# Kernel tuning notes

Measured on AMD Instinct MI355X. Metric: run time of the kernel, lower is better.

## Reference

```python
import jax, jax.numpy as jnp
import numpy as np

# ---- static config (seq_lens / is_prefill are Python lists in the original) ----
HIDDEN, H, D = 4096, 32, 128
SEQ = 1024            # prefill length / decode history length
N_PRE, N_DEC = 4, 4
T = N_PRE * SEQ + N_DEC            # 4100 total tokens
SEQ_LENS = [SEQ] * N_PRE + [SEQ] * N_DEC
IS_PREFILL = [True] * N_PRE + [False] * N_DEC
NUM_SLOTS = 8192
MAX_LEN, ROPE_BASE = 8192, 10000.0
SCALE = D ** -0.5


def _rope_tables():
    inv_freq = 1.0 / (ROPE_BASE ** (np.arange(0, D, 2, dtype=np.float32) / D))
    t = np.arange(MAX_LEN, dtype=np.float32)
    freqs = np.outer(t, inv_freq)
    emb = np.concatenate([freqs, freqs], axis=-1)  # [MAX_LEN, D]
    return jnp.asarray(np.cos(emb), jnp.float32), jnp.asarray(np.sin(emb), jnp.float32)

COS_T, SIN_T = _rope_tables()


def rotate_half(x):
    x1, x2 = jnp.split(x, 2, axis=-1)
    return jnp.concatenate([-x2, x1], axis=-1)


def setup_inputs() -> dict:
    key = jax.random.key(0)
    k1, k2, k3 = jax.random.split(key, 3)
    x = jax.random.normal(k1, (T, HIDDEN), jnp.float32)
    # positions: prefill seqs get 0..SEQ-1, decode seqs are at position SEQ
    pos = np.concatenate([np.tile(np.arange(SEQ), N_PRE), np.full(N_DEC, SEQ)]).astype(np.int64)
    positions = jnp.asarray(pos)
    slot_mapping = jnp.arange(T, dtype=jnp.int64)
    k_cache = jnp.zeros((NUM_SLOTS, H, D), jnp.float32)
    v_cache = jnp.zeros((NUM_SLOTS, H, D), jnp.float32)
    w_qkv = jax.random.normal(k2, (HIDDEN, 3 * H * D), jnp.float32) * 0.02
    w_out = jax.random.normal(k3, (H * D, HIDDEN), jnp.float32) * 0.02
    return {"x": x, "k_cache": k_cache, "v_cache": v_cache, "w_qkv": w_qkv,
            "w_out": w_out, "positions": positions, "slot_mapping": slot_mapping}


def reference(x, k_cache, v_cache, w_qkv, w_out, positions, slot_mapping):
    qkv = x @ w_qkv                                   # [T, 3*H*D]
    q, k, v = jnp.split(qkv, 3, axis=-1)
    q = q.reshape(T, H, D)
    k = k.reshape(T, H, D)
    v = v.reshape(T, H, D)
    cos = COS_T[positions][:, None, :]                # [T, 1, D]
    sin = SIN_T[positions][:, None, :]
    q = q * cos + rotate_half(q) * sin
    k = k * cos + rotate_half(k) * sin
    # scatter new k/v into flat paged cache
    kc = k_cache.at[slot_mapping].set(k)
    vc = v_cache.at[slot_mapping].set(v)

    outs = []
    off = 0
    for seq_len, prefill in zip(SEQ_LENS, IS_PREFILL):
        nq = seq_len if prefill else 1
        q_i = q[off:off + nq]                         # [nq, H, D]
        if prefill:
            k_i, v_i = k[off:off + nq], v[off:off + nq]
            attn = jnp.einsum('qhd,khd->hqk', q_i, k_i) * SCALE
            mask = jnp.triu(jnp.full((nq, nq), -jnp.inf, jnp.float32), 1)
            attn = jax.nn.softmax(attn + mask, axis=-1)
            out = jnp.einsum('hqk,khd->qhd', attn, v_i).reshape(nq, H * D)
        else:
            k_h, v_h = kc[:seq_len], vc[:seq_len]     # history from cache
            attn = jnp.einsum('qhd,khd->hqk', q_i, k_h) * SCALE
            attn = jax.nn.softmax(attn, axis=-1)
            out = jnp.einsum('hqk,khd->qhd', attn, v_h).reshape(1, H * D)
        outs.append(out)
        off += nq
    return jnp.concatenate(outs, axis=0) @ w_out      # [T, HIDDEN]
```

## Files before the change

### kernel.cpp

```cpp
#include <hip/hip_runtime.h>

#define T_TOK 4100
#define MMAIN 4096
#define HID   4096
#define NH    32
#define DH    128
#define NQKV  12288
#define ATT_SCALE 0.08838834764831845f
#define NEG_BIG  (-3.0e38f)

typedef unsigned short ushort_t;
typedef __attribute__((ext_vector_type(8))) short bf16x8;
typedef __attribute__((ext_vector_type(4))) float f32x4;

typedef const void __attribute__((address_space(1)))* gas_ptr;
typedef void __attribute__((address_space(3)))* las_ptr;

__device__ __forceinline__ ushort_t f2bf(float f){
  unsigned int u = __builtin_bit_cast(unsigned int, f);
  u = u + 0x7FFFu + ((u >> 16) & 1u);
  return (ushort_t)(u >> 16);
}
__device__ __forceinline__ float bf2f(ushort_t h){
  unsigned int u = ((unsigned int)h) << 16;
  return __builtin_bit_cast(float, u);
}
__device__ __forceinline__ f32x4 mfma16(bf16x8 a, bf16x8 b, f32x4 c){
  return __builtin_amdgcn_mfma_f32_16x16x32_bf16(a, b, c, 0, 0, 0);
}
__device__ __forceinline__ void gload_lds16(const void* g, void* l){
  __builtin_amdgcn_global_load_lds((gas_ptr)g, (las_ptr)l, 16, 0, 0);
}


__global__ void convert_x(const float* __restrict__ x, ushort_t* __restrict__ xb){
  const long i4 = (long)blockIdx.x * 256 + threadIdx.x;
  if (i4 >= (long)T_TOK * HID / 4) return;
  const long i = i4 * 4;
  const float4 v = *(const float4*)(x + i);
  union { ushort_t u[4]; uint2 w; } o;
  o.u[0] = f2bf(v.x); o.u[1] = f2bf(v.y); o.u[2] = f2bf(v.z); o.u[3] = f2bf(v.w);
  *(uint2*)(xb + i) = o.w;
}

__global__ void tconv(const float* __restrict__ W, ushort_t* __restrict__ WT, int R, int C){
  __shared__ float tile[32][33];
  const int bc = blockIdx.x, br = blockIdx.y;
  const int tid = threadIdx.x;
  const int cl = tid & 31, rl = tid >> 5;
  const long c = (long)bc * 32 + cl;
#pragma unroll
  for (int j = 0; j < 32; j += 8)
    tile[rl + j][cl] = W[((long)br * 32 + rl + j) * C + c];
  __syncthreads();
#pragma unroll
  for (int j = 0; j < 32; j += 8)
    WT[((long)bc * 32 + rl + j) * R + (long)br * 32 + cl] = f2bf(tile[cl][rl + j]);
}


#define MFMAQ(QM,QN,BARR)                                                         \
  _Pragma("unroll")                                                               \
  for (int mi = 0; mi < 4; ++mi) {                                                \
    _Pragma("unroll")                                                             \
    for (int ni = 0; ni < 2; ++ni) {                                              \
      acc[QM][QN][mi][ni] = mfma16(af[mi][0], BARR[ni][0], acc[QM][QN][mi][ni]);  \
      acc[QM][QN][mi][ni] = mfma16(af[mi][1], BARR[ni][1], acc[QM][QN][mi][ni]);  \
    } }

template<bool OUT_BF16>
__global__ void __launch_bounds__(512, 2)
gemm256(const ushort_t* __restrict__ A, const ushort_t* __restrict__ B,
        ushort_t* __restrict__ Cb, float* __restrict__ Cf,
        int N, int K, int GM, int Mvalid)
{
  extern __shared__ char smem[];
  char* smA = smem;
  char* smB = smem + 65536;

  const int nwg = gridDim.x;
  int bid = blockIdx.x;
  bid = (bid & 7) * (nwg >> 3) + (bid >> 3);
  const int bm = bid % GM, bn = bid / GM;

  const int tid = threadIdx.x;
  const int wid = tid >> 6, lane = tid & 63;
  const int wm = wid >> 2, wn = wid & 3;
  const int l16 = lane & 15, g = lane >> 4;
  const int lr = lane >> 3, lu = lane & 7;

  const long arow0 = (long)bm * 256;
  const long brow0 = (long)bn * 256;

  const ushort_t* aS[4]; const ushort_t* bS[4];
#pragma unroll
  for (int cc = 0; cc < 4; ++cc){
    aS[cc] = A + (arow0 + cc*64 + wid*8 + lr) * (long)K + (lu ^ lr) * 8;
    bS[cc] = B + (brow0 + cc*64 + wid*8 + lr) * (long)K + (lu ^ lr) * 8;
  }

  auto stageA = [&](int buf, int cc, long kt){
    gload_lds16(aS[cc] + kt, smA + buf*32768 + (cc*64 + wid*8)*128);
  };
  auto stageB = [&](int buf, int cc, long kt){
    gload_lds16(bS[cc] + kt, smB + buf*32768 + (cc*64 + wid*8)*128);
  };
  auto ldA = [&](int buf, int qm, int mi, int ks) -> bf16x8 {
    const int row = qm*128 + wm*64 + mi*16 + l16;
    return *(const bf16x8*)(smA + buf*32768 + row*128 + (((ks*4+g) ^ (l16&7))*16));
  };
  auto ldB = [&](int buf, int qn, int ni, int ks) -> bf16x8 {
    const int row = qn*128 + wn*32 + ni*16 + l16;
    return *(const bf16x8*)(smB + buf*32768 + row*128 + (((ks*4+g) ^ (l16&7))*16));
  };

  f32x4 acc[2][2][4][2];
#pragma unroll
  for (int a_ = 0; a_ < 2; ++a_)
#pragma unroll
  for (int b_ = 0; b_ < 2; ++b_)
#pragma unroll
  for (int c_ = 0; c_ < 4; ++c_)
#pragma unroll
  for (int d_ = 0; d_ < 2; ++d_) acc[a_][b_][c_][d_] = (f32x4){0.f,0.f,0.f,0.f};

  bf16x8 af[4][2], bf0[2][2], bf1[2][2];
  const int NT = K >> 6;

  stageA(0,0,0); stageA(0,1,0);
  stageB(0,0,0); stageB(0,1,0);
  stageB(0,2,0); stageB(0,3,0);
  stageA(0,2,0); stageA(0,3,0);
  asm volatile("s_waitcnt vmcnt(4)" ::: "memory");
  __builtin_amdgcn_s_barrier();

  auto tile = [&](int buf, long ktn){
    asm volatile("s_waitcnt vmcnt(2)" ::: "memory");
#pragma unroll
    for (int mi = 0; mi < 4; ++mi){ af[mi][0] = ldA(buf,0,mi,0); af[mi][1] = ldA(buf,0,mi,1); }
#pragma unroll
    for (int ni = 0; ni < 2; ++ni){ bf0[ni][0] = ldB(buf,0,ni,0); bf0[ni][1] = ldB(buf,0,ni,1); }
    stageA(buf^1, 0, ktn); stageA(buf^1, 1, ktn);
    __builtin_amdgcn_s_barrier();
    asm volatile("s_waitcnt lgkmcnt(0)" ::: "memory");
    __builtin_amdgcn_sched_barrier(0);
    __builtin_amdgcn_s_setprio(1);
    MFMAQ(0,0,bf0);
    __builtin_amdgcn_s_setprio(0);
    asm volatile("s_waitcnt vmcnt(2)" ::: "memory");
#pragma unroll
    for (int ni = 0; ni < 2; ++ni){ bf1[ni][0] = ldB(buf,1,ni,0); bf1[ni][1] = ldB(buf,1,ni,1); }
    stageB(buf^1, 0, ktn); stageB(buf^1, 1, ktn);
    __builtin_amdgcn_s_barrier();
    asm volatile("s_waitcnt lgkmcnt(0)" ::: "memory");
    __builtin_amdgcn_sched_barrier(0);
    __builtin_amdgcn_s_setprio(1);
    MFMAQ(0,1,bf1);
    __builtin_amdgcn_s_setprio(0);
#pragma unroll
    for (int mi = 0; mi < 4; ++mi){ af[mi][0] = ldA(buf,1,mi,0); af[mi][1] = ldA(buf,1,mi,1); }
    stageB(buf^1, 2, ktn); stageB(buf^1, 3, ktn);
    __builtin_amdgcn_s_barrier();
    asm volatile("s_waitcnt lgkmcnt(0)" ::: "memory");
    __builtin_amdgcn_sched_barrier(0);
    __builtin_amdgcn_s_setprio(1);
    MFMAQ(1,1,bf1);
    __builtin_amdgcn_s_setprio(0);
    asm volatile("s_waitcnt vmcnt(2)" ::: "memory");
    stageA(buf^1, 2, ktn); stageA(buf^1, 3, ktn);
    __builtin_amdgcn_s_barrier();
    __builtin_amdgcn_sched_barrier(0);
    __builtin_amdgcn_s_setprio(1);
    MFMAQ(1,0,bf0);
    __builtin_amdgcn_s_setprio(0);
  };

  for (int t = 0; t < NT; t += 2){
    const long k1 = (long)(t+1) * 64;
    const long k2 = (long)((t+2 < NT) ? (t+2) : (NT-1)) * 64;
    tile(0, k1);
    tile(1, k2);
  }
  asm volatile("s_waitcnt vmcnt(0)" ::: "memory");

#pragma unroll
  for (int qm = 0; qm < 2; ++qm)
#pragma unroll
  for (int qn = 0; qn < 2; ++qn)
#pragma unroll
  for (int mi = 0; mi < 4; ++mi)
#pragma unroll
  for (int ni = 0; ni < 2; ++ni)
#pragma unroll
  for (int r = 0; r < 4; ++r){
    const long row = arow0 + qm*128 + wm*64 + mi*16 + g*4 + r;
    const long col = brow0 + qn*128 + wn*32 + ni*16 + l16;
    if (OUT_BF16){
      Cb[row * N + col] = f2bf(acc[qm][qn][mi][ni][r]);
    } else {
      if (row < Mvalid) Cf[row * N + col] = acc[qm][qn][mi][ni][r];
    }
  }
}


__global__ void __launch_bounds__(256, 8)
gemv_tail(const ushort_t* __restrict__ A, const ushort_t* __restrict__ B,
          ushort_t* __restrict__ Cb, float* __restrict__ Cf, int ldc)
{
  const int col  = blockIdx.x * 4 + (threadIdx.x >> 6);
  const int lane = threadIdx.x & 63;
  const ushort_t* brow  = B + (long)col * HID + lane * 64;
  const ushort_t* abase = A + 4096L * HID + lane * 64;
  float acc0 = 0.f, acc1 = 0.f, acc2 = 0.f, acc3 = 0.f;
#pragma unroll
  for (int i = 0; i < 8; ++i){
    union { bf16x8 v; short s[8]; } bv, a0, a1, a2, a3;
    bv.v = *(const bf16x8*)(brow + i*8);
    a0.v = *(const bf16x8*)(abase + 0L*HID + i*8);
    a1.v = *(const bf16x8*)(abase + 1L*HID + i*8);
    a2.v = *(const bf16x8*)(abase + 2L*HID + i*8);
    a3.v = *(const bf16x8*)(abase + 3L*HID + i*8);
#pragma unroll
    for (int e = 0; e < 8; ++e){
      const float bf_ = bf2f((ushort_t)bv.s[e]);
      acc0 += bf2f((ushort_t)a0.s[e]) * bf_;
      acc1 += bf2f((ushort_t)a1.s[e]) * bf_;
      acc2 += bf2f((ushort_t)a2.s[e]) * bf_;
      acc3 += bf2f((ushort_t)a3.s[e]) * bf_;
    }
  }
#pragma unroll
  for (int off = 32; off; off >>= 1){
    acc0 += __shfl_xor(acc0, off);
    acc1 += __shfl_xor(acc1, off);
    acc2 += __shfl_xor(acc2, off);
    acc3 += __shfl_xor(acc3, off);
  }
  if (lane == 0){
    if (Cb){
      Cb[4096L*ldc + col] = f2bf(acc0);
      Cb[4097L*ldc + col] = f2bf(acc1);
      Cb[4098L*ldc + col] = f2bf(acc2);
      Cb[4099L*ldc + col] = f2bf(acc3);
    } else {
      Cf[4096L*ldc + col] = acc0;
      Cf[4097L*ldc + col] = acc1;
      Cf[4098L*ldc + col] = acc2;
      Cf[4099L*ldc + col] = acc3;
    }
  }
}


__global__ void rope_scatter(ushort_t* __restrict__ qkv,
                             const int* __restrict__ pos32,
                             const int* __restrict__ slot32,
                             ushort_t* __restrict__ kcw, ushort_t* __restrict__ vcw)
{
  const long gi = (long)blockIdx.x * 256 + threadIdx.x;
  if (gi >= (long)T_TOK * NH * 64) return;
  const int  i = gi & 63;
  const int  h = (gi >> 6) & 31;
  const long t = gi >> 11;

  const bool p64 = (pos32[1] == 0);
  const bool s64 = (slot32[1] == 0);
  const long pv   = p64 ? ((const long long*)pos32)[t]  : (long)pos32[t];
  const long slot = s64 ? ((const long long*)slot32)[t] : (long)slot32[t];

  const float inv = exp2f(-(float)i * 0.2076187116f);
  const float ang = (float)pv * inv;
  float sn, cs;
  __sincosf(ang, &sn, &cs);

  ushort_t* base = qkv + t * (long)NQKV + h * DH + i;
  const float q1 = bf2f(base[0]), q2 = bf2f(base[64]);
  base[0]  = f2bf(q1 * cs - q2 * sn);
  base[64] = f2bf(q2 * cs + q1 * sn);

  if (t < 4096){
    ushort_t* kb = base + HID;
    const float k1 = bf2f(kb[0]), k2 = bf2f(kb[64]);
    const float k1n = k1 * cs - k2 * sn, k2n = k2 * cs + k1 * sn;
    kb[0]  = f2bf(k1n);
    kb[64] = f2bf(k2n);

    if (slot >= 0 && slot < 1024){
      ushort_t* kd = kcw + (slot * NH + h) * DH + i;
      kd[0] = f2bf(k1n); kd[64] = f2bf(k2n);
      const ushort_t* vsrc = base + 2 * HID;
      ushort_t* vd = vcw + (slot * NH + h) * DH + i;
      vd[0] = vsrc[0]; vd[64] = vsrc[64];
    }
  }
}


__global__ void __launch_bounds__(256, 3)
attn_fused(const ushort_t* __restrict__ qkv, const ushort_t* __restrict__ kcw,
           const ushort_t* __restrict__ vcw, ushort_t* __restrict__ attn)
{
  __shared__ char sm[44032];
  const int qb = blockIdx.x, h = blockIdx.y, sq = blockIdx.z;
  const int tid = threadIdx.x, wid = tid >> 6, lane = tid & 63;

  if (qb == 16){
    float* qs  = (float*)sm;
    float* ps  = qs + 128;
    float* red = ps + 1024;
    float* oh  = red + 8;
    const long t = 4096 + sq;
    if (tid < 128) qs[tid] = bf2f(qkv[t * (long)NQKV + h*DH + tid]);
    __syncthreads();
    float sv[4];
#pragma unroll
    for (int j = 0; j < 4; j++){
      const int key = tid + j*256;
      const ushort_t* kr = kcw + ((long)key * NH + h) * DH;
      float acc = 0.f;
      for (int d = 0; d < 128; d += 8){
        union { bf16x8 v; short s[8]; } uu;
        uu.v = *(const bf16x8*)(kr + d);
#pragma unroll
        for (int e = 0; e < 8; e++) acc += qs[d+e] * bf2f((ushort_t)uu.s[e]);
      }
      sv[j] = acc * ATT_SCALE;
    }
    float mx = fmaxf(fmaxf(sv[0], sv[1]), fmaxf(sv[2], sv[3]));
#pragma unroll
    for (int off = 1; off < 64; off <<= 1) mx = fmaxf(mx, __shfl_xor(mx, off));
    if (lane == 0) red[wid] = mx;
    __syncthreads();
    const float gmax = fmaxf(fmaxf(red[0], red[1]), fmaxf(red[2], red[3]));
    float psum = 0.f;
#pragma unroll
    for (int j = 0; j < 4; j++){
      const float p = __expf(sv[j] - gmax);
      ps[tid + j*256] = p;
      psum += p;
    }
#pragma unroll
    for (int off = 1; off < 64; off <<= 1) psum += __shfl_xor(psum, off);
    if (lane == 0) red[4 + wid] = psum;
    __syncthreads();
    const float gsum = red[4] + red[5] + red[6] + red[7];
    const int d = tid & 127, half = tid >> 7;
    float acc = 0.f;
    for (int key = half*512; key < half*512 + 512; ++key)
      acc += ps[key] * bf2f(vcw[((long)key * NH + h) * DH + d]);
    if (half) oh[d] = acc;
    __syncthreads();
    if (!half) attn[t * HID + h*DH + d] = f2bf((acc + oh[d]) / gsum);
    return;
  }

  ushort_t (*Ks)[128]    = (ushort_t(*)[128])sm;
  ushort_t (*Vt)[72]     = (ushort_t(*)[72])(sm + 16384);
  ushort_t (*Ps)[16][72] = (ushort_t(*)[16][72])(sm + 34816);
  const long tok0 = (long)sq * 1024;
  const int l16 = lane & 15, g = lane >> 4;
  const int q0 = qb * 64;

  bf16x8 qf[4];
  {
    const ushort_t* qrow = qkv + (tok0 + q0 + wid*16 + l16) * (long)NQKV + h * DH;
#pragma unroll
    for (int dc = 0; dc < 4; ++dc) qf[dc] = *(const bf16x8*)(qrow + dc*32 + g*8);
  }

  f32x4 oacc[8];
#pragma unroll
  for (int i = 0; i < 8; i++) oacc[i] = (f32x4){0.f, 0.f, 0.f, 0.f};
  float mrow[4] = {NEG_BIG, NEG_BIG, NEG_BIG, NEG_BIG};
  float lrow[4] = {0.f, 0.f, 0.f, 0.f};

  const int nkb = qb + 1;
  for (int kb = 0; kb < nkb; ++kb){
    __syncthreads();
    {
      const ushort_t* kbase = qkv + (tok0 + kb*64) * (long)NQKV + HID + h * DH;
#pragma unroll
      for (int c = 0; c < 4; ++c){
        const int row = c*16 + wid*4 + g;
        const int pu = (l16 & 8) | ((l16 ^ (row & 7)) & 7);
        gload_lds16(kbase + (long)row * NQKV + pu*8, &Ks[c*16 + wid*4][0]);
      }
    }
    {
      const int key4 = (tid & 15) * 4;
      const int dg8  = tid >> 4;
      const ushort_t* vbase = qkv + (tok0 + kb*64) * (long)NQKV + 2*HID + h*DH + dg8*8;
      union { bf16x8 v; short s[8]; } vr[4];
#pragma unroll
      for (int j = 0; j < 4; ++j)
        vr[j].v = *(const bf16x8*)(vbase + (long)(key4 + j) * NQKV);
#pragma unroll
      for (int e = 0; e < 8; ++e){
        union { ushort_t u[4]; uint2 w; } o;
        o.u[0] = (ushort_t)vr[0].s[e]; o.u[1] = (ushort_t)vr[1].s[e];
        o.u[2] = (ushort_t)vr[2].s[e]; o.u[3] = (ushort_t)vr[3].s[e];
        *(uint2*)&Vt[dg8*8 + e][key4] = o.w;
      }
    }
    __syncthreads();

    {
      f32x4 sfr[4];
#pragma unroll
      for (int nf = 0; nf < 4; ++nf) sfr[nf] = (f32x4){0.f,0.f,0.f,0.f};
#pragma unroll
      for (int nf = 0; nf < 4; ++nf){
#pragma unroll
        for (int dc = 0; dc < 4; ++dc){
          const int uu = dc*4 + g;
          const int pu = (uu & 8) | ((uu ^ (l16 & 7)) & 7);
          bf16x8 kf = *(const bf16x8*)&Ks[nf*16 + l16][pu * 8];
          sfr[nf] = mfma16(qf[dc], kf, sfr[nf]);
        }
      }
      const bool diag = (kb == qb);
      float alpha[4];
#pragma unroll
      for (int r = 0; r < 4; r++){
        float s[4];
#pragma unroll
        for (int nf = 0; nf < 4; ++nf) s[nf] = sfr[nf][r] * ATT_SCALE;
        if (diag){
          const int qg = q0 + wid*16 + g*4 + r;
#pragma unroll
          for (int nf = 0; nf < 4; ++nf)
            if (kb*64 + nf*16 + l16 > qg) s[nf] = NEG_BIG;
        }
        float mx = fmaxf(fmaxf(s[0], s[1]), fmaxf(s[2], s[3]));
        mx = fmaxf(mx, __shfl_xor(mx, 1));
        mx = fmaxf(mx, __shfl_xor(mx, 2));
        mx = fmaxf(mx, __shfl_xor(mx, 4));
        mx = fmaxf(mx, __shfl_xor(mx, 8));
        const float mn = fmaxf(mrow[r], mx);
        const float al = __expf(mrow[r] - mn);
        float p[4], rs = 0.f;
#pragma unroll
        for (int nf = 0; nf < 4; ++nf){ p[nf] = __expf(s[nf] - mn); rs += p[nf]; }
        rs += __shfl_xor(rs, 1);
        rs += __shfl_xor(rs, 2);
        rs += __shfl_xor(rs, 4);
        rs += __shfl_xor(rs, 8);
        lrow[r] = lrow[r] * al + rs;
        mrow[r] = mn;
        alpha[r] = al;
#pragma unroll
        for (int nf = 0; nf < 4; ++nf)
          Ps[wid][g*4 + r][nf*16 + l16] = f2bf(p[nf]);
      }
#pragma unroll
      for (int df = 0; df < 8; ++df){
        f32x4 o = oacc[df];
        o[0] *= alpha[0]; o[1] *= alpha[1]; o[2] *= alpha[2]; o[3] *= alpha[3];
        oacc[df] = o;
      }
#pragma unroll
      for (int ks = 0; ks < 2; ++ks){
        bf16x8 pa = *(const bf16x8*)&Ps[wid][l16][ks*32 + g*8];
#pragma unroll
        for (int df = 0; df < 8; ++df){
          bf16x8 vf = *(const bf16x8*)&Vt[df*16 + l16][ks*32 + g*8];
          oacc[df] = mfma16(pa, vf, oacc[df]);
        }
      }
    }
  }

#pragma unroll
  for (int df = 0; df < 8; ++df){
#pragma unroll
    for (int r = 0; r < 4; ++r){
      const long row = tok0 + q0 + wid*16 + g*4 + r;
      attn[row * HID + h*DH + df*16 + l16] = f2bf(oacc[df][r] / lrow[r]);
    }
  }
}


extern "C" void kernel_launch(void* const* d_in, const int* in_sizes, int n_in,
                              void* d_out, int out_size, void* d_ws, size_t ws_size,
                              hipStream_t stream) {
  const float* x      = (const float*)d_in[0];
  const float* wqkv   = (const float*)d_in[3];
  const float* wout   = (const float*)d_in[4];
  const int*   pos    = (const int*)d_in[5];
  const int*   slots  = (const int*)d_in[6];

  char* ws = (char*)d_ws;
  ushort_t* xb    = (ushort_t*)(ws);
  ushort_t* qkvb  = (ushort_t*)(ws + 35651584L);
  ushort_t* wqkvT = (ushort_t*)(ws + 142606336L);
  ushort_t* attnb = (ushort_t*)(ws + 142606336L);
  ushort_t* woutT = (ushort_t*)(ws + 243269632L);
  ushort_t* kcw   = (ushort_t*)(ws + 276824064L);
  ushort_t* vcw   = (ushort_t*)(ws + 285212672L);

  hipFuncSetAttribute((const void*)gemm256<true>,
                      hipFuncAttributeMaxDynamicSharedMemorySize, 131072);
  hipFuncSetAttribute((const void*)gemm256<false>,
                      hipFuncAttributeMaxDynamicSharedMemorySize, 131072);

  convert_x<<<16400, 256, 0, stream>>>(x, xb);
  tconv<<<dim3(NQKV/32, HID/32), 256, 0, stream>>>(wqkv, wqkvT, HID, NQKV);
  tconv<<<dim3(HID/32, HID/32), 256, 0, stream>>>(wout, woutT, HID, HID);

  gemm256<true><<<(MMAIN/256)*(NQKV/256), 512, 131072, stream>>>(
      xb, wqkvT, qkvb, nullptr, NQKV, HID, MMAIN/256, MMAIN);
  gemv_tail<<<HID/4, 256, 0, stream>>>(xb, wqkvT, qkvb, nullptr, NQKV);

  rope_scatter<<<32800, 256, 0, stream>>>(qkvb, pos, slots, kcw, vcw);

  attn_fused<<<dim3(17, NH, 4), 256, 0, stream>>>(qkvb, kcw, vcw, attnb);

  gemm256<false><<<(MMAIN/256)*(HID/256), 512, 131072, stream>>>(
      attnb, woutT, nullptr, (float*)d_out, HID, HID, MMAIN/256, MMAIN);
  gemv_tail<<<HID/4, 256, 0, stream>>>(attnb, woutT, nullptr, (float*)d_out, HID);

  (void)in_sizes; (void)n_in; (void)out_size; (void)ws_size;
}
```

Baseline: 837.3 us.

## Double-buffer K/V tiles in attention and schedule longest query blocks first

The prefill attention loop now double-buffers K and V tiles in shared memory. The next tile's K is loaded asynchronously into LDS and its V is held in registers while the current tile's MFMAs run, which cuts the loop to one barrier per iteration. Query blocks are reversed (qb = 15 - bx) so the blocks with the most causal work are dispatched first, to reduce tail imbalance. The kernel moves to dynamic shared memory of about 77 KB and launch bounds drop from 3 to 2 blocks per CU, trading occupancy for overlap.

Result: no change. 847.9 us (+1.3%).

```diff
diff --git a/kernel.cpp b/kernel.cpp
--- a/kernel.cpp
+++ b/kernel.cpp
@@ -297,15 +297,15 @@
 }
 
 
-__global__ void __launch_bounds__(256, 3)
+__global__ void __launch_bounds__(256, 2)
 attn_fused(const ushort_t* __restrict__ qkv, const ushort_t* __restrict__ kcw,
            const ushort_t* __restrict__ vcw, ushort_t* __restrict__ attn)
 {
-  __shared__ char sm[44032];
-  const int qb = blockIdx.x, h = blockIdx.y, sq = blockIdx.z;
+  extern __shared__ char sm[];
+  const int bx = blockIdx.x, h = blockIdx.y, sq = blockIdx.z;
   const int tid = threadIdx.x, wid = tid >> 6, lane = tid & 63;
 
-  if (qb == 16){
+  if (bx == 16){
     float* qs  = (float*)sm;
     float* ps  = qs + 128;
     float* red = ps + 1024;
@@ -355,12 +355,14 @@
     return;
   }
 
-  ushort_t (*Ks)[128]    = (ushort_t(*)[128])sm;
-  ushort_t (*Vt)[72]     = (ushort_t(*)[72])(sm + 16384);
-  ushort_t (*Ps)[16][72] = (ushort_t(*)[16][72])(sm + 34816);
+  char* smKs = sm;
+  char* smVt = sm + 32768;
+  char* smPs = sm + 69632;
+  const int qb = 15 - bx;
   const long tok0 = (long)sq * 1024;
   const int l16 = lane & 15, g = lane >> 4;
   const int q0 = qb * 64;
+  const int key4 = (tid & 15) * 4, dg8 = tid >> 4;
 
   bf16x8 qf[4];
   {
@@ -369,106 +371,115 @@
     for (int dc = 0; dc < 4; ++dc) qf[dc] = *(const bf16x8*)(qrow + dc*32 + g*8);
   }
 
+  auto Kstage = [&](int kb, int buf){
+    const ushort_t* kbase = qkv + (tok0 + kb*64) * (long)NQKV + HID + h * DH;
+#pragma unroll
+    for (int c = 0; c < 4; ++c){
+      const int row = c*16 + wid*4 + g;
+      const int pu = (l16 & 8) | ((l16 ^ (row & 7)) & 7);
+      gload_lds16(kbase + (long)row * NQKV + pu*8, smKs + buf*16384 + (c*16 + wid*4)*256);
+    }
+  };
+  bf16x8 vreg[4];
+  auto Vload = [&](int kb){
+    const ushort_t* vbase = qkv + (tok0 + kb*64) * (long)NQKV + 2*HID + h*DH + dg8*8;
+#pragma unroll
+    for (int j = 0; j < 4; ++j)
+      vreg[j] = *(const bf16x8*)(vbase + (long)(key4 + j) * NQKV);
+  };
+  auto Vwrite = [&](int buf){
+    union { bf16x8 v; short s[8]; } vr[4];
+#pragma unroll
+    for (int j = 0; j < 4; ++j) vr[j].v = vreg[j];
+#pragma unroll
+    for (int e = 0; e < 8; ++e){
+      union { ushort_t u[4]; uint2 w; } o;
+      o.u[0] = (ushort_t)vr[0].s[e]; o.u[1] = (ushort_t)vr[1].s[e];
+      o.u[2] = (ushort_t)vr[2].s[e]; o.u[3] = (ushort_t)vr[3].s[e];
+      *(uint2*)(smVt + buf*18432 + ((dg8*8 + e)*72 + key4)*2) = o.w;
+    }
+  };
+
   f32x4 oacc[8];
 #pragma unroll
   for (int i = 0; i < 8; i++) oacc[i] = (f32x4){0.f, 0.f, 0.f, 0.f};
   float mrow[4] = {NEG_BIG, NEG_BIG, NEG_BIG, NEG_BIG};
   float lrow[4] = {0.f, 0.f, 0.f, 0.f};
 
-  const int nkb = qb + 1;
-  for (int kb = 0; kb < nkb; ++kb){
+  Kstage(0, 0);
+  Vload(0);
+  Vwrite(0);
+  __syncthreads();
+
+  for (int kb = 0; kb <= qb; ++kb){
+    const int buf = kb & 1;
+    if (kb < qb){ Kstage(kb + 1, buf ^ 1); Vload(kb + 1); }
+
+    f32x4 sfr[4];
+#pragma unroll
+    for (int nf = 0; nf < 4; ++nf) sfr[nf] = (f32x4){0.f,0.f,0.f,0.f};
+#pragma unroll
+    for (int nf = 0; nf < 4; ++nf){
+#pragma unroll
+      for (int dc = 0; dc < 4; ++dc){
+        const int uu = dc*4 + g;
+        const int pu = (uu & 8) | ((uu ^ (l16 & 7)) & 7);
+        bf16x8 kf = *(const bf16x8*)(smKs + buf*16384 + (nf*16 + l16)*256 + pu*16);
+        sfr[nf] = mfma16(qf[dc], kf, sfr[nf]);
+      }
+    }
+    const bool diag = (kb == qb);
+    float alpha[4];
+#pragma unroll
+    for (int r = 0; r < 4; r++){
+      float s[4];
+#pragma unroll
+      for (int nf = 0; nf < 4; ++nf) s[nf] = sfr[nf][r] * ATT_SCALE;
+      if (diag){
+        const int qg = q0 + wid*16 + g*4 + r;
+#pragma unroll
+        for (int nf = 0; nf < 4; ++nf)
+          if (kb*64 + nf*16 + l16 > qg) s[nf] = NEG_BIG;
+      }
+      float mx = fmaxf(fmaxf(s[0], s[1]), fmaxf(s[2], s[3]));
+      mx = fmaxf(mx, __shfl_xor(mx, 1));
+      mx = fmaxf(mx, __shfl_xor(mx, 2));
+      mx = fmaxf(mx, __shfl_xor(mx, 4));
+      mx = fmaxf(mx, __shfl_xor(mx, 8));
+      const float mn = fmaxf(mrow[r], mx);
+      const float al = __expf(mrow[r] - mn);
+      float p[4], rs = 0.f;
+#pragma unroll
+      for (int nf = 0; nf < 4; ++nf){ p[nf] = __expf(s[nf] - mn); rs += p[nf]; }
+      rs += __shfl_xor(rs, 1);
+      rs += __shfl_xor(rs, 2);
+      rs += __shfl_xor(rs, 4);
+      rs += __shfl_xor(rs, 8);
+      lrow[r] = lrow[r] * al + rs;
+      mrow[r] = mn;
+      alpha[r] = al;
+#pragma unroll
+      for (int nf = 0; nf < 4; ++nf)
+        *(ushort_t*)(smPs + ((wid*16 + g*4 + r)*72 + nf*16 + l16)*2) = f2bf(p[nf]);
+    }
+#pragma unroll
+    for (int df = 0; df < 8; ++df){
+      f32x4 o = oacc[df];
+      o[0] *= alpha[0]; o[1] *= alpha[1]; o[2] *= alpha[2]; o[3] *= alpha[3];
+      oacc[df] = o;
+    }
+#pragma unroll
+    for (int ks = 0; ks < 2; ++ks){
+      bf16x8 pa = *(const bf16x8*)(smPs + ((wid*16 + l16)*72 + ks*32 + g*8)*2);
+#pragma unroll
+      for (int df = 0; df < 8; ++df){
+        bf16x8 vf = *(const bf16x8*)(smVt + buf*18432 + ((df*16 + l16)*72 + ks*32 + g*8)*2);
+        oacc[df] = mfma16(pa, vf, oacc[df]);
+      }
+    }
+
+    if (kb < qb) Vwrite(buf ^ 1);
     __syncthreads();
-    {
-      const ushort_t* kbase = qkv + (tok0 + kb*64) * (long)NQKV + HID + h * DH;
-#pragma unroll
-      for (int c = 0; c < 4; ++c){
-        const int row = c*16 + wid*4 + g;
-        const int pu = (l16 & 8) | ((l16 ^ (row & 7)) & 7);
-        gload_lds16(kbase + (long)row * NQKV + pu*8, &Ks[c*16 + wid*4][0]);
-      }
-    }
-    {
-      const int key4 = (tid & 15) * 4;
-      const int dg8  = tid >> 4;
-      const ushort_t* vbase = qkv + (tok0 + kb*64) * (long)NQKV + 2*HID + h*DH + dg8*8;
-      union { bf16x8 v; short s[8]; } vr[4];
-#pragma unroll
-      for (int j = 0; j < 4; ++j)
-        vr[j].v = *(const bf16x8*)(vbase + (long)(key4 + j) * NQKV);
-#pragma unroll
-      for (int e = 0; e < 8; ++e){
-        union { ushort_t u[4]; uint2 w; } o;
-        o.u[0] = (ushort_t)vr[0].s[e]; o.u[1] = (ushort_t)vr[1].s[e];
-        o.u[2] = (ushort_t)vr[2].s[e]; o.u[3] = (ushort_t)vr[3].s[e];
-        *(uint2*)&Vt[dg8*8 + e][key4] = o.w;
-      }
-    }
-    __syncthreads();
-
-    {
-      f32x4 sfr[4];
-#pragma unroll
-      for (int nf = 0; nf < 4; ++nf) sfr[nf] = (f32x4){0.f,0.f,0.f,0.f};
-#pragma unroll
-      for (int nf = 0; nf < 4; ++nf){
-#pragma unroll
-        for (int dc = 0; dc < 4; ++dc){
-          const int uu = dc*4 + g;
-          const int pu = (uu & 8) | ((uu ^ (l16 & 7)) & 7);
-          bf16x8 kf = *(const bf16x8*)&Ks[nf*16 + l16][pu * 8];
-          sfr[nf] = mfma16(qf[dc], kf, sfr[nf]);
-        }
-      }
-      const bool diag = (kb == qb);
-      float alpha[4];
-#pragma unroll
-      for (int r = 0; r < 4; r++){
-        float s[4];
-#pragma unroll
-        for (int nf = 0; nf < 4; ++nf) s[nf] = sfr[nf][r] * ATT_SCALE;
-        if (diag){
-          const int qg = q0 + wid*16 + g*4 + r;
-#pragma unroll
-          for (int nf = 0; nf < 4; ++nf)
-            if (kb*64 + nf*16 + l16 > qg) s[nf] = NEG_BIG;
-        }
-        float mx = fmaxf(fmaxf(s[0], s[1]), fmaxf(s[2], s[3]));
-        mx = fmaxf(mx, __shfl_xor(mx, 1));
-        mx = fmaxf(mx, __shfl_xor(mx, 2));
-        mx = fmaxf(mx, __shfl_xor(mx, 4));
-        mx = fmaxf(mx, __shfl_xor(mx, 8));
-        const float mn = fmaxf(mrow[r], mx);
-        const float al = __expf(mrow[r] - mn);
-        float p[4], rs = 0.f;
-#pragma unroll
-        for (int nf = 0; nf < 4; ++nf){ p[nf] = __expf(s[nf] - mn); rs += p[nf]; }
-        rs += __shfl_xor(rs, 1);
-        rs += __shfl_xor(rs, 2);
-        rs += __shfl_xor(rs, 4);
-        rs += __shfl_xor(rs, 8);
-        lrow[r] = lrow[r] * al + rs;
-        mrow[r] = mn;
-        alpha[r] = al;
-#pragma unroll
-        for (int nf = 0; nf < 4; ++nf)
-          Ps[wid][g*4 + r][nf*16 + l16] = f2bf(p[nf]);
-      }
-#pragma unroll
-      for (int df = 0; df < 8; ++df){
-        f32x4 o = oacc[df];
-        o[0] *= alpha[0]; o[1] *= alpha[1]; o[2] *= alpha[2]; o[3] *= alpha[3];
-        oacc[df] = o;
-      }
-#pragma unroll
-      for (int ks = 0; ks < 2; ++ks){
-        bf16x8 pa = *(const bf16x8*)&Ps[wid][l16][ks*32 + g*8];
-#pragma unroll
-        for (int df = 0; df < 8; ++df){
-          bf16x8 vf = *(const bf16x8*)&Vt[df*16 + l16][ks*32 + g*8];
-          oacc[df] = mfma16(pa, vf, oacc[df]);
-        }
-      }
-    }
   }
 
 #pragma unroll
@@ -504,6 +515,8 @@
                       hipFuncAttributeMaxDynamicSharedMemorySize, 131072);
   hipFuncSetAttribute((const void*)gemm256<false>,
                       hipFuncAttributeMaxDynamicSharedMemorySize, 131072);
+  hipFuncSetAttribute((const void*)attn_fused,
+                      hipFuncAttributeMaxDynamicSharedMemorySize, 78848);
 
   convert_x<<<16400, 256, 0, stream>>>(x, xb);
   tconv<<<dim3(NQKV/32, HID/32), 256, 0, stream>>>(wqkv, wqkvT, HID, NQKV);
@@ -515,7 +528,7 @@
 
   rope_scatter<<<32800, 256, 0, stream>>>(qkvb, pos, slots, kcw, vcw);
 
-  attn_fused<<<dim3(17, NH, 4), 256, 0, stream>>>(qkvb, kcw, vcw, attnb);
+  attn_fused<<<dim3(17, NH, 4), 256, 78848, stream>>>(qkvb, kcw, vcw, attnb);
 
   gemm256<false><<<(MMAIN/256)*(HID/256), 512, 131072, stream>>>(
       attnb, woutT, nullptr, (float*)d_out, HID, HID, MMAIN/256, MMAIN);
```

## Widen attention query tile to 128 rows with 512-thread blocks and K/V reuse

Applied to the files above, without the earlier changes.

The prefill attention kernel now processes 128 query rows per block with 8 waves, so each staged 64-key K/V tile is shared by twice as many queries, roughly halving global K/V loads. Blocks are launched in reverse (heaviest-first) order, waves skip key tiles entirely above their causal diagonal, and s_setprio is raised around the MFMA sections. Shared memory becomes dynamic and sized for the larger P buffer. The decode path is adapted to 512 threads. The trade-offs are lower occupancy, idle waves on diagonal tiles, and fewer blocks in the grid.

Result: slower. 870.7 us (+4.0%).

```diff
diff --git a/kernel.cpp b/kernel.cpp
--- a/kernel.cpp
+++ b/kernel.cpp
@@ -297,26 +297,26 @@
 }
 
 
-__global__ void __launch_bounds__(256, 3)
+__global__ void __launch_bounds__(512, 2)
 attn_fused(const ushort_t* __restrict__ qkv, const ushort_t* __restrict__ kcw,
            const ushort_t* __restrict__ vcw, ushort_t* __restrict__ attn)
 {
-  __shared__ char sm[44032];
-  const int qb = blockIdx.x, h = blockIdx.y, sq = blockIdx.z;
+  extern __shared__ char sm[];
+  const int bx = blockIdx.x, h = blockIdx.y, sq = blockIdx.z;
   const int tid = threadIdx.x, wid = tid >> 6, lane = tid & 63;
 
-  if (qb == 16){
+  if (bx == 8){
     float* qs  = (float*)sm;
     float* ps  = qs + 128;
     float* red = ps + 1024;
-    float* oh  = red + 8;
+    float* oh  = red + 16;
     const long t = 4096 + sq;
     if (tid < 128) qs[tid] = bf2f(qkv[t * (long)NQKV + h*DH + tid]);
     __syncthreads();
-    float sv[4];
-#pragma unroll
-    for (int j = 0; j < 4; j++){
-      const int key = tid + j*256;
+    float sv[2];
+#pragma unroll
+    for (int j = 0; j < 2; j++){
+      const int key = tid + j*512;
       const ushort_t* kr = kcw + ((long)key * NH + h) * DH;
       float acc = 0.f;
       for (int d = 0; d < 128; d += 8){
@@ -327,44 +327,51 @@
       }
       sv[j] = acc * ATT_SCALE;
     }
-    float mx = fmaxf(fmaxf(sv[0], sv[1]), fmaxf(sv[2], sv[3]));
+    float mx = fmaxf(sv[0], sv[1]);
 #pragma unroll
     for (int off = 1; off < 64; off <<= 1) mx = fmaxf(mx, __shfl_xor(mx, off));
     if (lane == 0) red[wid] = mx;
     __syncthreads();
-    const float gmax = fmaxf(fmaxf(red[0], red[1]), fmaxf(red[2], red[3]));
+    float gmax = red[0];
+#pragma unroll
+    for (int w = 1; w < 8; ++w) gmax = fmaxf(gmax, red[w]);
     float psum = 0.f;
 #pragma unroll
-    for (int j = 0; j < 4; j++){
+    for (int j = 0; j < 2; j++){
       const float p = __expf(sv[j] - gmax);
-      ps[tid + j*256] = p;
+      ps[tid + j*512] = p;
       psum += p;
     }
 #pragma unroll
     for (int off = 1; off < 64; off <<= 1) psum += __shfl_xor(psum, off);
-    if (lane == 0) red[4 + wid] = psum;
+    if (lane == 0) red[8 + wid] = psum;
     __syncthreads();
-    const float gsum = red[4] + red[5] + red[6] + red[7];
-    const int d = tid & 127, half = tid >> 7;
+    float gsum = red[8];
+#pragma unroll
+    for (int w = 1; w < 8; ++w) gsum += red[8 + w];
+    const int d = tid & 127, q4 = tid >> 7;
     float acc = 0.f;
-    for (int key = half*512; key < half*512 + 512; ++key)
+    for (int key = q4*256; key < q4*256 + 256; ++key)
       acc += ps[key] * bf2f(vcw[((long)key * NH + h) * DH + d]);
-    if (half) oh[d] = acc;
+    if (q4) oh[(q4-1)*128 + d] = acc;
     __syncthreads();
-    if (!half) attn[t * HID + h*DH + d] = f2bf((acc + oh[d]) / gsum);
+    if (!q4) attn[t * HID + h*DH + d] = f2bf((acc + oh[d] + oh[128+d] + oh[256+d]) / gsum);
     return;
   }
 
-  ushort_t (*Ks)[128]    = (ushort_t(*)[128])sm;
-  ushort_t (*Vt)[72]     = (ushort_t(*)[72])(sm + 16384);
-  ushort_t (*Ps)[16][72] = (ushort_t(*)[16][72])(sm + 34816);
+  char* smKs = sm;
+  char* smVt = sm + 16384;
+  char* smPs = sm + 34816;
+  const int qb = 7 - bx;
   const long tok0 = (long)sq * 1024;
   const int l16 = lane & 15, g = lane >> 4;
-  const int q0 = qb * 64;
+  const int q0 = qb * 128;
+  const int q0w = q0 + wid*16;
+  const int key2 = (tid & 31) * 2, dg8 = tid >> 5;
 
   bf16x8 qf[4];
   {
-    const ushort_t* qrow = qkv + (tok0 + q0 + wid*16 + l16) * (long)NQKV + h * DH;
+    const ushort_t* qrow = qkv + (tok0 + q0w + l16) * (long)NQKV + h * DH;
 #pragma unroll
     for (int dc = 0; dc < 4; ++dc) qf[dc] = *(const bf16x8*)(qrow + dc*32 + g*8);
   }
@@ -375,51 +382,50 @@
   float mrow[4] = {NEG_BIG, NEG_BIG, NEG_BIG, NEG_BIG};
   float lrow[4] = {0.f, 0.f, 0.f, 0.f};
 
-  const int nkb = qb + 1;
+  const int nkb = 2*qb + 2;
   for (int kb = 0; kb < nkb; ++kb){
     __syncthreads();
     {
       const ushort_t* kbase = qkv + (tok0 + kb*64) * (long)NQKV + HID + h * DH;
 #pragma unroll
-      for (int c = 0; c < 4; ++c){
-        const int row = c*16 + wid*4 + g;
+      for (int c = 0; c < 2; ++c){
+        const int row = c*32 + wid*4 + g;
         const int pu = (l16 & 8) | ((l16 ^ (row & 7)) & 7);
-        gload_lds16(kbase + (long)row * NQKV + pu*8, &Ks[c*16 + wid*4][0]);
+        gload_lds16(kbase + (long)row * NQKV + pu*8, smKs + (c*32 + wid*4)*256);
       }
     }
     {
-      const int key4 = (tid & 15) * 4;
-      const int dg8  = tid >> 4;
       const ushort_t* vbase = qkv + (tok0 + kb*64) * (long)NQKV + 2*HID + h*DH + dg8*8;
-      union { bf16x8 v; short s[8]; } vr[4];
-#pragma unroll
-      for (int j = 0; j < 4; ++j)
-        vr[j].v = *(const bf16x8*)(vbase + (long)(key4 + j) * NQKV);
+      union { bf16x8 v; short s[8]; } vr[2];
+#pragma unroll
+      for (int j = 0; j < 2; ++j)
+        vr[j].v = *(const bf16x8*)(vbase + (long)(key2 + j) * NQKV);
 #pragma unroll
       for (int e = 0; e < 8; ++e){
-        union { ushort_t u[4]; uint2 w; } o;
+        union { ushort_t u[2]; unsigned w; } o;
         o.u[0] = (ushort_t)vr[0].s[e]; o.u[1] = (ushort_t)vr[1].s[e];
-        o.u[2] = (ushort_t)vr[2].s[e]; o.u[3] = (ushort_t)vr[3].s[e];
-        *(uint2*)&Vt[dg8*8 + e][key4] = o.w;
+        *(unsigned*)(smVt + ((dg8*8 + e)*72 + key2)*2) = o.w;
       }
     }
     __syncthreads();
 
-    {
+    if (kb*64 <= q0w + 15){
       f32x4 sfr[4];
 #pragma unroll
       for (int nf = 0; nf < 4; ++nf) sfr[nf] = (f32x4){0.f,0.f,0.f,0.f};
+      __builtin_amdgcn_s_setprio(1);
 #pragma unroll
       for (int nf = 0; nf < 4; ++nf){
 #pragma unroll
         for (int dc = 0; dc < 4; ++dc){
           const int uu = dc*4 + g;
           const int pu = (uu & 8) | ((uu ^ (l16 & 7)) & 7);
-          bf16x8 kf = *(const bf16x8*)&Ks[nf*16 + l16][pu * 8];
+          bf16x8 kf = *(const bf16x8*)(smKs + (nf*16 + l16)*256 + pu*16);
           sfr[nf] = mfma16(qf[dc], kf, sfr[nf]);
         }
       }
-      const bool diag = (kb == qb);
+      __builtin_amdgcn_s_setprio(0);
+      const bool diag = (kb*64 + 63 > q0w);
       float alpha[4];
 #pragma unroll
       for (int r = 0; r < 4; r++){
@@ -427,7 +433,7 @@
 #pragma unroll
         for (int nf = 0; nf < 4; ++nf) s[nf] = sfr[nf][r] * ATT_SCALE;
         if (diag){
-          const int qg = q0 + wid*16 + g*4 + r;
+          const int qg = q0w + g*4 + r;
 #pragma unroll
           for (int nf = 0; nf < 4; ++nf)
             if (kb*64 + nf*16 + l16 > qg) s[nf] = NEG_BIG;
@@ -451,7 +457,7 @@
         alpha[r] = al;
 #pragma unroll
         for (int nf = 0; nf < 4; ++nf)
-          Ps[wid][g*4 + r][nf*16 + l16] = f2bf(p[nf]);
+          *(ushort_t*)(smPs + ((wid*16 + g*4 + r)*72 + nf*16 + l16)*2) = f2bf(p[nf]);
       }
 #pragma unroll
       for (int df = 0; df < 8; ++df){
@@ -459,15 +465,17 @@
         o[0] *= alpha[0]; o[1] *= alpha[1]; o[2] *= alpha[2]; o[3] *= alpha[3];
         oacc[df] = o;
       }
+      __builtin_amdgcn_s_setprio(1);
 #pragma unroll
       for (int ks = 0; ks < 2; ++ks){
-        bf16x8 pa = *(const bf16x8*)&Ps[wid][l16][ks*32 + g*8];
+        bf16x8 pa = *(const bf16x8*)(smPs + ((wid*16 + l16)*72 + ks*32 + g*8)*2);
 #pragma unroll
         for (int df = 0; df < 8; ++df){
-          bf16x8 vf = *(const bf16x8*)&Vt[df*16 + l16][ks*32 + g*8];
+          bf16x8 vf = *(const bf16x8*)(smVt + ((df*16 + l16)*72 + ks*32 + g*8)*2);
           oacc[df] = mfma16(pa, vf, oacc[df]);
         }
       }
+      __builtin_amdgcn_s_setprio(0);
     }
   }
 
@@ -475,7 +483,7 @@
   for (int df = 0; df < 8; ++df){
 #pragma unroll
     for (int r = 0; r < 4; ++r){
-      const long row = tok0 + q0 + wid*16 + g*4 + r;
+      const long row = tok0 + q0w + g*4 + r;
       attn[row * HID + h*DH + df*16 + l16] = f2bf(oacc[df][r] / lrow[r]);
     }
   }
@@ -504,6 +512,8 @@
                       hipFuncAttributeMaxDynamicSharedMemorySize, 131072);
   hipFuncSetAttribute((const void*)gemm256<false>,
                       hipFuncAttributeMaxDynamicSharedMemorySize, 131072);
+  hipFuncSetAttribute((const void*)attn_fused,
+                      hipFuncAttributeMaxDynamicSharedMemorySize, 53248);
 
   convert_x<<<16400, 256, 0, stream>>>(x, xb);
   tconv<<<dim3(NQKV/32, HID/32), 256, 0, stream>>>(wqkv, wqkvT, HID, NQKV);
@@ -515,7 +525,7 @@
 
   rope_scatter<<<32800, 256, 0, stream>>>(qkvb, pos, slots, kcw, vcw);
 
-  attn_fused<<<dim3(17, NH, 4), 256, 0, stream>>>(qkvb, kcw, vcw, attnb);
+  attn_fused<<<dim3(9, NH, 4), 512, 53248, stream>>>(qkvb, kcw, vcw, attnb);
 
   gemm256<false><<<(MMAIN/256)*(HID/256), 512, 131072, stream>>>(
       attnb, woutT, nullptr, (float*)d_out, HID, HID, MMAIN/256, MMAIN);
```
